# Kernel tuning notes

Measured on AMD Instinct MI355X. Metric: run time of the kernel, lower is better.

Reference implementation:

```python
import jax, jax.numpy as jnp
import numpy as np

N_QUBITS = 10
N_LATENT = 6
N_LAYERS = 2
AMP_DIM = 2 ** N_QUBITS  # 1024


def _apply_1q(state, gate, q):
    # state: [B] + [2]*N_QUBITS complex; gate: [2,2]; wire q -> axis q+1 (wire 0 = MSB)
    s = jnp.tensordot(gate, state, axes=[[1], [q + 1]])  # new axis at front
    return jnp.moveaxis(s, 0, q + 1)


def _ry_mat(theta):
    c = jnp.cos(theta / 2)
    s = jnp.sin(theta / 2)
    return jnp.stack([jnp.stack([c, -s]), jnp.stack([s, c])]).astype(jnp.complex64)


def _rz_mat(theta):
    half = theta / 2
    e = jnp.cos(half) + 1j * jnp.sin(half)  # e^{i theta/2}
    zero = jnp.zeros((), jnp.complex64)
    return jnp.stack([jnp.stack([jnp.conj(e), zero]), jnp.stack([zero, e])]).astype(jnp.complex64)


def _cnot(state, c, t):
    # flip target axis where control bit == 1
    ctrl_shape = [1] * (N_QUBITS + 1)
    ctrl_shape[c + 1] = 2
    ctrl = jnp.arange(2).reshape(ctrl_shape)
    return jnp.where(ctrl == 1, jnp.flip(state, axis=t + 1), state)


def _expvals(state):
    # PauliX, PauliY, PauliZ on wires 0..N_LATENT-1  -> [B, 3*N_LATENT]
    rest = tuple(range(1, N_QUBITS))  # axes of the 9 remaining wires after a take
    xs, ys, zs = [], [], []
    for q in range(N_LATENT):
        s0 = jnp.take(state, 0, axis=q + 1)
        s1 = jnp.take(state, 1, axis=q + 1)
        z01 = jnp.conj(s0) * s1
        xs.append(2.0 * jnp.sum(z01.real, axis=rest))
        ys.append(2.0 * jnp.sum(z01.imag, axis=rest))
        zs.append(jnp.sum(jnp.abs(s0) ** 2 - jnp.abs(s1) ** 2, axis=rest))
    return jnp.stack(xs + ys + zs, axis=1)


def _simulate(x, weights):
    B, D = x.shape
    if D < AMP_DIM:
        x = jnp.pad(x, ((0, 0), (0, AMP_DIM - D)))
    else:
        x = x[:, :AMP_DIM]
    norm = jnp.maximum(jnp.linalg.norm(x, axis=-1, keepdims=True), 1e-8)
    x = x / norm
    state = x.astype(jnp.complex64).reshape((B,) + (2,) * N_QUBITS)
    for layer in range(N_LAYERS):
        off = layer * N_QUBITS * 3
        for q in range(N_QUBITS):
            state = _apply_1q(state, _ry_mat(weights[off + q]), q)
        for q in range(N_QUBITS):
            state = _apply_1q(state, _rz_mat(weights[off + N_QUBITS + q]), q)
        for q in range(N_QUBITS):
            state = _cnot(state, q, (q + 1) % N_QUBITS)
        for q in range(N_QUBITS):
            state = _apply_1q(state, _ry_mat(weights[off + 2 * N_QUBITS + q]), q)
    return _expvals(state).astype(jnp.float32)


def setup_inputs() -> dict:
    key = jax.random.key(0)
    k1, k2 = jax.random.split(key)
    B, D = 32768, 768
    x = jax.random.normal(k1, (B, D), dtype=jnp.float32)
    std = np.sqrt(2.0 / (N_QUBITS + N_LAYERS)).astype(np.float32)
    weights = jax.random.normal(k2, (N_LAYERS * N_QUBITS * 3,), dtype=jnp.float32) * std
    return {"x": x, "weights": weights}


def reference(x, weights):
    return _simulate(x, weights)
```

## Files before the change

### kernel.cpp

```cpp
#include <hip/hip_runtime.h>

#define DIN 768

typedef float f2 __attribute__((ext_vector_type(2)));
typedef int i2v __attribute__((ext_vector_type(2)));

#if __has_builtin(__builtin_amdgcn_permlane32_swap)
#define HAVE_PL32 1
#endif
#if __has_builtin(__builtin_amdgcn_permlane16_swap)
#define HAVE_PL16 1
#endif

__device__ __forceinline__ int f2i(float v) { return __builtin_bit_cast(int, v); }
__device__ __forceinline__ float i2f(int v) { return __builtin_bit_cast(float, v); }

template<int CTRL>
__device__ __forceinline__ float dppf(float v) {
  const int i = f2i(v);
  return i2f(__builtin_amdgcn_update_dpp(i, i, CTRL, 0xF, 0xF, true));
}
template<int CTRL>
__device__ __forceinline__ f2 dppf2(f2 v) {
  f2 r; r.x = dppf<CTRL>(v.x); r.y = dppf<CTRL>(v.y); return r;
}

__device__ __forceinline__ f2 wsum2(f2 v) {
  v += dppf2<0xB1>(v);
  v += dppf2<0x4E>(v);
  v += dppf2<0x124>(v);
  v += dppf2<0x128>(v);
#ifdef HAVE_PL16
  { i2v rx = __builtin_amdgcn_permlane16_swap(f2i(v.x), f2i(v.x), false, false);
    i2v ry = __builtin_amdgcn_permlane16_swap(f2i(v.y), f2i(v.y), false, false);
    v.x = i2f(rx.x) + i2f(rx.y);
    v.y = i2f(ry.x) + i2f(ry.y); }
#else
  v.x += __shfl_xor(v.x, 16); v.y += __shfl_xor(v.y, 16);
#endif
#ifdef HAVE_PL32
  { i2v rx = __builtin_amdgcn_permlane32_swap(f2i(v.x), f2i(v.x), false, false);
    i2v ry = __builtin_amdgcn_permlane32_swap(f2i(v.y), f2i(v.y), false, false);
    v.x = i2f(rx.x) + i2f(rx.y);
    v.y = i2f(ry.x) + i2f(ry.y); }
#else
  v.x += __shfl_xor(v.x, 32); v.y += __shfl_xor(v.y, 32);
#endif
  return v;
}

template<int MASK>
__device__ __forceinline__ f2 shflx_f2(f2 v, int lane) {
  f2 r;
  if constexpr (MASK == 1) {
    r = dppf2<0xB1>(v);
  } else if constexpr (MASK == 2) {
    r = dppf2<0x4E>(v);
  } else if constexpr (MASK == 16) {
#ifdef HAVE_PL16
    const i2v a = __builtin_amdgcn_permlane16_swap(f2i(v.x), f2i(v.x), false, false);
    const i2v b = __builtin_amdgcn_permlane16_swap(f2i(v.y), f2i(v.y), false, false);
    const bool hi = (lane >> 4) & 1;
    r.x = hi ? i2f(a.x) : i2f(a.y);
    r.y = hi ? i2f(b.x) : i2f(b.y);
#else
    r.x = __shfl_xor(v.x, 16); r.y = __shfl_xor(v.y, 16);
#endif
  } else if constexpr (MASK == 32) {
#ifdef HAVE_PL32
    const i2v a = __builtin_amdgcn_permlane32_swap(f2i(v.x), f2i(v.x), false, false);
    const i2v b = __builtin_amdgcn_permlane32_swap(f2i(v.y), f2i(v.y), false, false);
    const bool lo = lane < 32;
    r.x = lo ? i2f(a.y) : i2f(a.x);
    r.y = lo ? i2f(b.y) : i2f(b.x);
#else
    r.x = __shfl_xor(v.x, 32); r.y = __shfl_xor(v.y, 32);
#endif
  } else {
    r.x = __shfl_xor(v.x, MASK); r.y = __shfl_xor(v.y, MASK);
  }
  return r;
}

__device__ __forceinline__ int swz(int i) { return i ^ ((i >> 4) & 31); }

__device__ __forceinline__ int cnotL(int i) {
  const int b9 = (i >> 9) & 1;
  const int b8 = (i >> 8) & 1;
  const int b0 = i & 1;
  return ((i ^ (i >> 1)) & 0xFF) | ((b8 ^ b9 ^ b0) << 8) | ((b9 ^ b0) << 9);
}

template<int RB>
__device__ __forceinline__ void ry1(f2 (&a)[16], float c, float s) {
#pragma unroll
  for (int r = 0; r < 16; ++r) {
    if (!(r & (1 << RB))) {
      const int p = r | (1 << RB);
      const f2 a0 = a[r], a1 = a[p];
      a[r] = a0 * c - a1 * s;
      a[p] = a1 * c + a0 * s;
    }
  }
}
template<int RB>
__device__ __forceinline__ void ry2(f2 (&re)[16], f2 (&im)[16], float c, float s) {
  ry1<RB>(re, c, s);
  ry1<RB>(im, c, s);
}
template<int MASK>
__device__ __forceinline__ void ry1_shfl(int lane, f2 (&a)[16], float c, float s) {
  const float ss = (lane & MASK) ? s : -s;
#pragma unroll
  for (int r = 0; r < 16; ++r) {
    const f2 p = shflx_f2<MASK>(a[r], lane);
    a[r] = a[r] * c + p * ss;
  }
}

template<int RB>
__device__ __forceinline__ void xyr(const f2 (&re)[16], const f2 (&im)[16], f2& aX, f2& aY) {
#pragma unroll
  for (int r = 0; r < 16; ++r) {
    if (!(r & (1 << RB))) {
      const int p = r | (1 << RB);
      aX += re[r] * re[p] + im[r] * im[p];
      aY += re[r] * im[p] - im[r] * re[p];
    }
  }
}
template<int MASK>
__device__ __forceinline__ void xys(int lane, const f2 (&re)[16], const f2 (&im)[16], f2& aX, f2& aY) {
  const float sgn = (lane & MASK) ? -1.f : 1.f;
#pragma unroll
  for (int r = 0; r < 16; ++r) {
    const f2 pr = shflx_f2<MASK>(re[r], lane);
    const f2 pi = shflx_f2<MASK>(im[r], lane);
    aX += re[r] * pr + im[r] * pi;
    aY += (re[r] * pi - im[r] * pr) * sgn;
  }
}

__global__ void qae_prep(const float* __restrict__ w, float2* __restrict__ ws) {
  const int i = threadIdx.x;
  if (i < 50) {
    float s, c; __sincosf(0.5f * w[i], &s, &c);
    ws[i] = make_float2(c, s);
  } else if (i < 56) {
    float s, c; __sincosf(w[i], &s, &c);
    ws[i] = make_float2(c, s);
  } else if (i < 60) {
    ws[i] = make_float2(1.f, 0.f);
  } else if (i < 70) {
    const int q = i - 60;
    float s, c; __sincosf(0.5f * (w[20 + q] + w[30 + q]), &s, &c);
    ws[i] = make_float2(c, s);
  }
  float p1 = 0.f, p2 = 0.f;
#pragma unroll
  for (int b = 0; b < 10; ++b) {
    const float sg = ((i >> b) & 1) ? 0.5f : -0.5f;
    p1 += sg * w[10 + 9 - b];
    p2 += sg * w[40 + 9 - b];
  }
  float s, c;
  __sincosf(p1, &s, &c); ws[70 + i]        = make_float2(c, s);
  __sincosf(p2, &s, &c); ws[70 + 1024 + i] = make_float2(c, s);
}

__global__ __launch_bounds__(128, 4) void qae_main(const float* __restrict__ x,
                                                   const float2* __restrict__ gt,
                                                   float* __restrict__ out, int Btot) {
  __shared__ f2 lds[2 * 1024];
  const int tid  = threadIdx.x;
  const int lane = tid & 63;
  const int wid  = tid >> 6;
  const int gw   = blockIdx.x * 2 + wid;
  const int b0   = gw * 2, b1 = b0 + 1;
  if (b0 >= Btot) return;
  const bool has1 = (b1 < Btot);
  f2* stc = lds + (wid << 10);
  const float2* rz1 = gt + 70;
  const float2* rz2 = gt + 70 + 1024;

  f2 g[16];
  f2 ss = (f2){0.f, 0.f};
  const float* x0 = x + (size_t)b0 * DIN;
  const float* x1 = x + (size_t)b1 * DIN;
#pragma unroll
  for (int t = 0; t < 4; ++t) {
    const int idx = lane * 16 + 4 * t;
    float4 va = make_float4(0.f, 0.f, 0.f, 0.f);
    float4 vb = make_float4(0.f, 0.f, 0.f, 0.f);
    if (idx < DIN) {
      va = *reinterpret_cast<const float4*>(x0 + idx);
      if (has1) vb = *reinterpret_cast<const float4*>(x1 + idx);
    }
    g[4*t+0] = (f2){va.x, vb.x}; g[4*t+1] = (f2){va.y, vb.y};
    g[4*t+2] = (f2){va.z, vb.z}; g[4*t+3] = (f2){va.w, vb.w};
#pragma unroll
    for (int k = 0; k < 4; ++k) ss += g[4*t+k] * g[4*t+k];
  }
  ss = wsum2(ss);
  const f2 inv = (f2){1.f / fmaxf(ss.x, 1e-16f), 1.f / fmaxf(ss.y, 1e-16f)};

  float2 cs;
  cs = gt[6]; ry1<3>(g, cs.x, cs.y);
  cs = gt[7]; ry1<2>(g, cs.x, cs.y);
  cs = gt[8]; ry1<1>(g, cs.x, cs.y);
  cs = gt[9]; ry1<0>(g, cs.x, cs.y);
  cs = gt[4]; ry1_shfl<2>(lane, g, cs.x, cs.y);
  cs = gt[5]; ry1_shfl<1>(lane, g, cs.x, cs.y);

#pragma unroll
  for (int r = 0; r < 16; ++r) stc[swz((lane << 4) | r)] = g[r];
#pragma unroll
  for (int r = 0; r < 16; ++r) g[r] = stc[swz((r << 6) | lane)];

  cs = gt[0]; ry1<3>(g, cs.x, cs.y);
  cs = gt[1]; ry1<2>(g, cs.x, cs.y);
  cs = gt[2]; ry1<1>(g, cs.x, cs.y);
  cs = gt[3]; ry1<0>(g, cs.x, cs.y);

  f2 re[16], im[16];
#pragma unroll
  for (int r = 0; r < 16; ++r) {
    const float2 t = rz1[(r << 6) | lane];
    re[r] = g[r] * t.x;
    im[r] = g[r] * t.y;
  }

#pragma unroll
  for (int r = 0; r < 16; ++r) stc[swz((r << 6) | lane)] = re[r];
#pragma unroll
  for (int r = 0; r < 16; ++r) re[r] = stc[swz(cnotL((lane << 4) | r))];
#pragma unroll
  for (int r = 0; r < 16; ++r) stc[swz((r << 6) | lane)] = im[r];
#pragma unroll
  for (int r = 0; r < 16; ++r) im[r] = stc[swz(cnotL((lane << 4) | r))];

  cs = gt[66]; ry2<3>(re, im, cs.x, cs.y);
  cs = gt[67]; ry2<2>(re, im, cs.x, cs.y);
  cs = gt[68]; ry2<1>(re, im, cs.x, cs.y);
  cs = gt[69]; ry2<0>(re, im, cs.x, cs.y);
  cs = gt[64]; ry1_shfl<2>(lane, re, cs.x, cs.y); ry1_shfl<2>(lane, im, cs.x, cs.y);
  cs = gt[65]; ry1_shfl<1>(lane, re, cs.x, cs.y); ry1_shfl<1>(lane, im, cs.x, cs.y);

#pragma unroll
  for (int r = 0; r < 16; ++r) stc[swz((lane << 4) | r)] = re[r];
#pragma unroll
  for (int r = 0; r < 16; ++r) re[r] = stc[swz((r << 6) | lane)];
#pragma unroll
  for (int r = 0; r < 16; ++r) stc[swz((lane << 4) | r)] = im[r];
#pragma unroll
  for (int r = 0; r < 16; ++r) im[r] = stc[swz((r << 6) | lane)];

  cs = gt[60]; ry2<3>(re, im, cs.x, cs.y);
  cs = gt[61]; ry2<2>(re, im, cs.x, cs.y);
  cs = gt[62]; ry2<1>(re, im, cs.x, cs.y);
  cs = gt[63]; ry2<0>(re, im, cs.x, cs.y);

#pragma unroll
  for (int r = 0; r < 16; ++r) {
    const float2 t = rz2[(r << 6) | lane];
    const f2 nre = re[r] * t.x - im[r] * t.y;
    im[r] = re[r] * t.y + im[r] * t.x;
    re[r] = nre;
  }

#pragma unroll
  for (int r = 0; r < 16; ++r) stc[swz((r << 6) | lane)] = re[r];
#pragma unroll
  for (int r = 0; r < 16; ++r) re[r] = stc[swz(cnotL((r << 6) | lane))];
#pragma unroll
  for (int r = 0; r < 16; ++r) stc[swz((r << 6) | lane)] = im[r];
#pragma unroll
  for (int r = 0; r < 16; ++r) im[r] = stc[swz(cnotL((r << 6) | lane))];

  f2 aX[6], aY[6], aZ[6];
#pragma unroll
  for (int q = 0; q < 6; ++q) { aX[q] = (f2){0.f,0.f}; aY[q] = (f2){0.f,0.f}; aZ[q] = (f2){0.f,0.f}; }

  {
    f2 psum = (f2){0.f, 0.f};
#pragma unroll
    for (int r = 0; r < 16; ++r) {
      const f2 p = re[r] * re[r] + im[r] * im[r];
      psum += p;
      aZ[0] += (r & 8) ? -p : p;
      aZ[1] += (r & 4) ? -p : p;
      aZ[2] += (r & 2) ? -p : p;
      aZ[3] += (r & 1) ? -p : p;
    }
    aZ[4] = ((lane >> 5) & 1) ? -psum : psum;
    aZ[5] = ((lane >> 4) & 1) ? -psum : psum;
  }

  xyr<3>(re, im, aX[0], aY[0]);
  xyr<2>(re, im, aX[1], aY[1]);
  xyr<1>(re, im, aX[2], aY[2]);
  xyr<0>(re, im, aX[3], aY[3]);
  xys<32>(lane, re, im, aX[4], aY[4]);
  xys<16>(lane, re, im, aX[5], aY[5]);

#pragma unroll
  for (int q = 0; q < 6; ++q) {
    aX[q] = wsum2(aX[q]);
    aY[q] = wsum2(aY[q]);
    aZ[q] = wsum2(aZ[q]);
  }

  f2 o[18];
#pragma unroll
  for (int q = 0; q < 6; ++q) {
    const float2 fa = gt[50 + q];
    const float fac = (q < 4) ? 2.f : 1.f;
    const f2 X = aX[q] * fac, Y = aY[q] * fac, Z = aZ[q];
    o[q]      = (X * fa.x + Z * fa.y) * inv;
    o[6 + q]  = Y * inv;
    o[12 + q] = (Z * fa.x - X * fa.y) * inv;
  }
  if (lane == 0) {
    float* ob = out + (size_t)b0 * 18;
#pragma unroll
    for (int k = 0; k < 18; ++k) ob[k] = o[k].x;
  } else if (lane == 1 && has1) {
    float* ob = out + (size_t)b1 * 18;
#pragma unroll
    for (int k = 0; k < 18; ++k) ob[k] = o[k].y;
  }
}

extern "C" void kernel_launch(void* const* d_in, const int* in_sizes, int n_in,
                              void* d_out, int out_size, void* d_ws, size_t ws_size,
                              hipStream_t stream) {
  const float* x = (const float*)d_in[0];
  const float* w = (const float*)d_in[1];
  float* out = (float*)d_out;
  float2* ws = (float2*)d_ws;
  const int B = in_sizes[0] / DIN;
  qae_prep<<<dim3(1), dim3(1024), 0, stream>>>(w, ws);
  const int grid = (B + 3) / 4;
  qae_main<<<dim3(grid), dim3(128), 0, stream>>>(x, (const float2*)ws, out, B);
}
```

Before: 124.7 us.

## Replace per-observable wave reductions with DPP quad reduce plus LDS transpose

The final expectation-value reduction is restructured. Each of 18 accumulators is reduced within quads via DPP, partial sums are written to LDS, and 36 lanes each finish one output by summing 16 partials, then write the output in parallel. This replaces 18 full-wave shuffle reductions and the serial 18-element stores from lanes 0 and 1. The occupancy hint is also dropped from launch_bounds, which changes the register budget and risks lower occupancy. The LDS reuse relies on wave-local ordering with no explicit barrier.

```diff
diff --git a/kernel.cpp b/kernel.cpp
--- a/kernel.cpp
+++ b/kernel.cpp
@@ -168,9 +168,9 @@
   __sincosf(p2, &s, &c); ws[70 + 1024 + i] = make_float2(c, s);
 }
 
-__global__ __launch_bounds__(128, 4) void qae_main(const float* __restrict__ x,
-                                                   const float2* __restrict__ gt,
-                                                   float* __restrict__ out, int Btot) {
+__global__ __launch_bounds__(128) void qae_main(const float* __restrict__ x,
+                                                const float2* __restrict__ gt,
+                                                float* __restrict__ out, int Btot) {
   __shared__ f2 lds[2 * 1024];
   const int tid  = threadIdx.x;
   const int lane = tid & 63;
@@ -277,57 +277,67 @@
 #pragma unroll
   for (int r = 0; r < 16; ++r) im[r] = stc[swz(cnotL((r << 6) | lane))];
 
-  f2 aX[6], aY[6], aZ[6];
-#pragma unroll
-  for (int q = 0; q < 6; ++q) { aX[q] = (f2){0.f,0.f}; aY[q] = (f2){0.f,0.f}; aZ[q] = (f2){0.f,0.f}; }
+  f2 a18[18];
+#pragma unroll
+  for (int k = 0; k < 12; ++k) a18[k] = (f2){0.f, 0.f};
 
   {
     f2 psum = (f2){0.f, 0.f};
+    f2 z0 = (f2){0.f,0.f}, z1 = (f2){0.f,0.f}, z2 = (f2){0.f,0.f}, z3 = (f2){0.f,0.f};
 #pragma unroll
     for (int r = 0; r < 16; ++r) {
       const f2 p = re[r] * re[r] + im[r] * im[r];
       psum += p;
-      aZ[0] += (r & 8) ? -p : p;
-      aZ[1] += (r & 4) ? -p : p;
-      aZ[2] += (r & 2) ? -p : p;
-      aZ[3] += (r & 1) ? -p : p;
-    }
-    aZ[4] = ((lane >> 5) & 1) ? -psum : psum;
-    aZ[5] = ((lane >> 4) & 1) ? -psum : psum;
-  }
-
-  xyr<3>(re, im, aX[0], aY[0]);
-  xyr<2>(re, im, aX[1], aY[1]);
-  xyr<1>(re, im, aX[2], aY[2]);
-  xyr<0>(re, im, aX[3], aY[3]);
-  xys<32>(lane, re, im, aX[4], aY[4]);
-  xys<16>(lane, re, im, aX[5], aY[5]);
-
-#pragma unroll
-  for (int q = 0; q < 6; ++q) {
-    aX[q] = wsum2(aX[q]);
-    aY[q] = wsum2(aY[q]);
-    aZ[q] = wsum2(aZ[q]);
-  }
-
-  f2 o[18];
-#pragma unroll
-  for (int q = 0; q < 6; ++q) {
-    const float2 fa = gt[50 + q];
-    const float fac = (q < 4) ? 2.f : 1.f;
-    const f2 X = aX[q] * fac, Y = aY[q] * fac, Z = aZ[q];
-    o[q]      = (X * fa.x + Z * fa.y) * inv;
-    o[6 + q]  = Y * inv;
-    o[12 + q] = (Z * fa.x - X * fa.y) * inv;
-  }
-  if (lane == 0) {
-    float* ob = out + (size_t)b0 * 18;
-#pragma unroll
-    for (int k = 0; k < 18; ++k) ob[k] = o[k].x;
-  } else if (lane == 1 && has1) {
-    float* ob = out + (size_t)b1 * 18;
-#pragma unroll
-    for (int k = 0; k < 18; ++k) ob[k] = o[k].y;
+      z0 += (r & 8) ? -p : p;
+      z1 += (r & 4) ? -p : p;
+      z2 += (r & 2) ? -p : p;
+      z3 += (r & 1) ? -p : p;
+    }
+    a18[12] = z0; a18[13] = z1; a18[14] = z2; a18[15] = z3;
+    a18[16] = ((lane >> 5) & 1) ? -psum : psum;
+    a18[17] = ((lane >> 4) & 1) ? -psum : psum;
+  }
+
+  xyr<3>(re, im, a18[0], a18[6]);
+  xyr<2>(re, im, a18[1], a18[7]);
+  xyr<1>(re, im, a18[2], a18[8]);
+  xyr<0>(re, im, a18[3], a18[9]);
+  xys<32>(lane, re, im, a18[4], a18[10]);
+  xys<16>(lane, re, im, a18[5], a18[11]);
+
+#pragma unroll
+  for (int k = 0; k < 18; ++k) {
+    f2 v = a18[k];
+    v += dppf2<0xB1>(v);
+    v += dppf2<0x4E>(v);
+    a18[k] = v;
+  }
+  float* red = reinterpret_cast<float*>(stc);
+  if ((lane & 3) == 0) {
+    const int q = lane >> 2;
+    f2* redf2 = reinterpret_cast<f2*>(red);
+#pragma unroll
+    for (int k = 0; k < 18; ++k) redf2[q * 18 + k] = a18[k];
+  }
+  if (lane < 36) {
+    const int c  = (lane >= 18) ? 1 : 0;
+    const int j  = lane - 18 * c;
+    const int jq = (j < 6) ? j : ((j < 12) ? j - 6 : j - 12);
+    const int jp = (j < 6) ? (j + 12) : ((j >= 12) ? (j - 12) : j);
+    float S = 0.f, P = 0.f;
+#pragma unroll
+    for (int q = 0; q < 16; ++q) {
+      S += red[(q * 18 + j ) * 2 + c];
+      P += red[(q * 18 + jp) * 2 + c];
+    }
+    const float fac  = (jq < 4) ? 2.f : 1.f;
+    const float2 fa  = gt[50 + jq];
+    const float invc = c ? inv.y : inv.x;
+    float o;
+    if (j < 6)       o = (fac * S * fa.x + P * fa.y) * invc;
+    else if (j < 12) o = fac * S * invc;
+    else             o = (S * fa.x - fac * P * fa.y) * invc;
+    if (c == 0 || has1) out[(size_t)(b0 + c) * 18 + j] = o;
   }
 }
 
```

After: 106.4 us. 1.17x faster.
